# Performance work log

Measured on AMD Instinct MI355X. Metric: run time of the kernel, lower is better.

## Reference

```python
import jax, jax.numpy as jnp
import numpy as np

N = 100000
E = 3200000
IN_CH, HID, OUT = 256, 64, 32


def setup_inputs() -> dict:
    key = jax.random.key(0)
    ks = jax.random.split(key, 8)
    x = jax.random.normal(ks[0], (N, IN_CH), dtype=jnp.float32)
    edge_index = jax.random.randint(ks[1], (2, E), 0, N, dtype=jnp.int64)
    # Glorot-ish init for weights, zeros for biases (PyG GCNConv: lin has no bias; conv bias added post-aggregation)
    W1 = jax.random.normal(ks[2], (IN_CH, HID), dtype=jnp.float32) / np.sqrt(IN_CH)
    b1 = jnp.zeros((HID,), dtype=jnp.float32)
    W2 = jax.random.normal(ks[3], (HID, OUT), dtype=jnp.float32) / np.sqrt(HID)
    b2 = jnp.zeros((OUT,), dtype=jnp.float32)
    Wc = jax.random.normal(ks[4], (OUT, 1), dtype=jnp.float32) / np.sqrt(OUT)
    bc = jnp.zeros((1,), dtype=jnp.float32)
    return {"x": x, "edge_index": edge_index, "W1": W1, "b1": b1,
            "W2": W2, "b2": b2, "Wc": Wc, "bc": bc}


def _gcn_norm(edge_index, num_nodes):
    # Add self-loops (PyG default), compute symmetric normalization D^{-1/2} A D^{-1/2}
    loops = jnp.arange(num_nodes, dtype=edge_index.dtype)
    row = jnp.concatenate([edge_index[0], loops])  # source
    col = jnp.concatenate([edge_index[1], loops])  # target (aggregation index)
    ones = jnp.ones(row.shape[0], dtype=jnp.float32)
    deg = jax.ops.segment_sum(ones, col, num_segments=num_nodes)
    dis = jnp.where(deg > 0, jax.lax.rsqrt(jnp.maximum(deg, 1e-12)), 0.0)
    norm = dis[row] * dis[col]  # [E+N]
    return row, col, norm


def _gcn_conv(x, W, b, row, col, norm, num_nodes):
    h = x @ W                                   # [N, F_out] dense transform first
    msg = h[row] * norm[:, None]                # gather + scale per edge
    agg = jax.ops.segment_sum(msg, col, num_segments=num_nodes)
    return agg + b


def reference(x, edge_index, W1, b1, W2, b2, Wc, bc):
    num_nodes = x.shape[0]
    row, col, norm = _gcn_norm(edge_index, num_nodes)
    h = jax.nn.elu(_gcn_conv(x, W1, b1, row, col, norm, num_nodes))
    h = jax.nn.elu(_gcn_conv(h, W2, b2, row, col, norm, num_nodes))
    return (h @ Wc + bc)[:, 0]                  # squeeze(1) -> [N]
```

## Files before the change

kernel.cpp:

```cpp
#include <hip/hip_runtime.h>
#include <hip/hip_fp16.h>
#include <math.h>

#define N_NODES 100000
#define N_EDGES 3200000
#define IN_CH   256
#define HID     64
#define OUTC    32
#define BSHIFT  8
#define BNODES  256
#define NBUCK   ((N_NODES + BNODES - 1) / BNODES)
#define CHUNK   4096
#define EPT     16
#define CAP     9216

static constexpr size_t align256(size_t x) { return (x + 255) & ~(size_t)255; }
static constexpr size_t OFF_PTRB = 0;
static constexpr size_t OFF_PTRE = OFF_PTRB + align256((size_t)N_NODES * 4);
static constexpr size_t OFF_GCUR = OFF_PTRE + align256((size_t)N_NODES * 4);
static constexpr size_t OFF_DIS  = OFF_GCUR + align256((size_t)NBUCK * 4);
static constexpr size_t OFF_SRC  = OFF_DIS  + align256((size_t)N_NODES * 4);
static constexpr size_t OFF_PART = OFF_SRC  + align256((size_t)NBUCK * CAP * 4);
static constexpr size_t OFF_S1   = OFF_PART;
static constexpr size_t OFF_S2   = OFF_PART + align256((size_t)NBUCK * CAP * 4);

typedef _Float16 f16;
typedef f16 f16x8 __attribute__((ext_vector_type(8)));
typedef float f32x4 __attribute__((ext_vector_type(4)));

__device__ __forceinline__ void acc8(float* acc, float4 raw) {
    const __half2* hp = (const __half2*)&raw;
    float2 f0 = __half22float2(hp[0]);
    float2 f1 = __half22float2(hp[1]);
    float2 f2 = __half22float2(hp[2]);
    float2 f3 = __half22float2(hp[3]);
    acc[0] += f0.x; acc[1] += f0.y; acc[2] += f1.x; acc[3] += f1.y;
    acc[4] += f2.x; acc[5] += f2.y; acc[6] += f3.x; acc[7] += f3.y;
}

__global__ __launch_bounds__(256) void bucket_init(int* __restrict__ gcur) {
    int b = blockIdx.x * 256 + threadIdx.x;
    if (b < NBUCK) gcur[b] = b * CAP;
}

__global__ __launch_bounds__(256) void partition_edges(const int* __restrict__ row,
                                                       const int* __restrict__ col,
                                                       int* __restrict__ gcur,
                                                       int* __restrict__ part) {
    __shared__ int lhist[NBUCK];
    __shared__ int lbase[NBUCK];
    const int t  = threadIdx.x;
    const int e0 = blockIdx.x * CHUNK;
    for (int i = t; i < NBUCK; i += 256) lhist[i] = 0;
    __syncthreads();

    int pk[EPT], br[EPT];
#pragma unroll
    for (int i = 0; i < EPT; ++i) {
        int e = e0 + i * 256 + t;
        if (e < N_EDGES) {
            int d = col[e];
            int b = d >> BSHIFT;
            int r = atomicAdd(&lhist[b], 1);
            pk[i] = row[e] | ((d & (BNODES - 1)) << 17);
            br[i] = b | (r << 10);
        } else {
            br[i] = -1;
        }
    }
    __syncthreads();

    const int off = (int)((blockIdx.x * 131u) % NBUCK);
    for (int i = t; i < NBUCK; i += 256) {
        int bb = i + off;
        if (bb >= NBUCK) bb -= NBUCK;
        int c = lhist[bb];
        lbase[bb] = (c > 0) ? atomicAdd(&gcur[bb], c) : 0;
    }
    __syncthreads();

#pragma unroll
    for (int i = 0; i < EPT; ++i) {
        if (br[i] >= 0) {
            int b = br[i] & 1023;
            int r = br[i] >> 10;
            part[lbase[b] + r] = pk[i];
        }
    }
}

__global__ __launch_bounds__(256) void bucket_build(const int* __restrict__ gcur,
                                                    const int* __restrict__ part,
                                                    int* __restrict__ ptrb,
                                                    int* __restrict__ ptre,
                                                    float* __restrict__ dis,
                                                    int* __restrict__ srcs) {
    __shared__ int pcache[CAP];
    __shared__ int lh[BNODES];
    __shared__ int lb[BNODES];
    __shared__ int lcur[BNODES];
    __shared__ int ls[BNODES];
    const int b = blockIdx.x;
    const int t = threadIdx.x;
    lh[t] = 0; lcur[t] = 0;
    __syncthreads();
    const int cnt = gcur[b] - b * CAP;
    const size_t pbase = (size_t)b * CAP;

    for (int i = t; i < cnt; i += 256) {
        int p = part[pbase + i];
        pcache[i] = p;
        atomicAdd(&lh[p >> 17], 1);
    }
    __syncthreads();

    int val = lh[t];
    ls[t] = val;
    __syncthreads();
    for (int off = 1; off < BNODES; off <<= 1) {
        int add = (t >= off) ? ls[t - off] : 0;
        __syncthreads();
        ls[t] += add;
        __syncthreads();
    }
    lb[t] = ls[t] - val;
    __syncthreads();

    int v = b * BNODES + t;
    if (v < N_NODES) {
        ptrb[v] = b * CAP + lb[t];
        ptre[v] = b * CAP + lb[t] + val;
        dis[v]  = rsqrtf((float)val + 1.0f);
    }

    for (int i = t; i < cnt; i += 256) {
        int p    = pcache[i];
        int dlow = p >> 17;
        int src  = p & 0x1FFFF;
        int r    = atomicAdd(&lcur[dlow], 1);
        srcs[pbase + lb[dlow] + r] = src;
    }
}

__global__ __launch_bounds__(256) void gemm1(const float* __restrict__ x,
                                             const float* __restrict__ W1,
                                             const float* __restrict__ dis,
                                             __half* __restrict__ s1h) {
    __shared__ __align__(16) char lds_raw[30720];
    f16* xh  = (f16*)lds_raw;
    f16* xl  = (f16*)(lds_raw + 10240);
    f16* wth = (f16*)(lds_raw + 20480);
    f16* wtl = (f16*)(lds_raw + 25600);

    const int t    = threadIdx.x;
    const int row0 = blockIdx.x * 128;
    const int lane = t & 63;
    const int wv   = t >> 6;
    const int lr   = lane & 15;
    const int kg   = lane >> 4;

    f32x4 acc[2][4];
#pragma unroll
    for (int m = 0; m < 2; ++m)
#pragma unroll
        for (int n = 0; n < 4; ++n) acc[m][n] = (f32x4){0.f, 0.f, 0.f, 0.f};

    for (int kt = 0; kt < 8; ++kt) {
#pragma unroll
        for (int i = 0; i < 4; ++i) {
            int L  = i * 256 + t;
            int r  = L >> 3;
            int k4 = L & 7;
            int rg = row0 + r;
            float4 v = make_float4(0.f, 0.f, 0.f, 0.f);
            if (rg < N_NODES)
                v = ((const float4*)x)[(size_t)rg * 64 + kt * 8 + k4];
            union { f16 h[4]; unsigned long long u; } ph, pl;
            const float* vf = (const float*)&v;
#pragma unroll
            for (int c = 0; c < 4; ++c) {
                f16 hi = (f16)vf[c];
                ph.h[c] = hi;
                pl.h[c] = (f16)(vf[c] - (float)hi);
            }
            *(unsigned long long*)(&xh[r * 40 + k4 * 4]) = ph.u;
            *(unsigned long long*)(&xl[r * 40 + k4 * 4]) = pl.u;
        }
#pragma unroll
        for (int i = 0; i < 2; ++i) {
            int L  = i * 256 + t;
            int k  = L >> 4;
            int j4 = L & 15;
            float4 v = ((const float4*)W1)[(size_t)(kt * 32 + k) * 16 + j4];
            const float* vf = (const float*)&v;
#pragma unroll
            for (int c = 0; c < 4; ++c) {
                f16 hi = (f16)vf[c];
                wth[(j4 * 4 + c) * 40 + k] = hi;
                wtl[(j4 * 4 + c) * 40 + k] = (f16)(vf[c] - (float)hi);
            }
        }
        __syncthreads();

        f16x8 ah[2], al[2], bh[4], bl[4];
#pragma unroll
        for (int m = 0; m < 2; ++m) {
            ah[m] = *(const f16x8*)(&xh[(wv * 32 + m * 16 + lr) * 40 + kg * 8]);
            al[m] = *(const f16x8*)(&xl[(wv * 32 + m * 16 + lr) * 40 + kg * 8]);
        }
#pragma unroll
        for (int n = 0; n < 4; ++n) {
            bh[n] = *(const f16x8*)(&wth[(n * 16 + lr) * 40 + kg * 8]);
            bl[n] = *(const f16x8*)(&wtl[(n * 16 + lr) * 40 + kg * 8]);
        }
#pragma unroll
        for (int m = 0; m < 2; ++m)
#pragma unroll
            for (int n = 0; n < 4; ++n) {
                acc[m][n] = __builtin_amdgcn_mfma_f32_16x16x32_f16(ah[m], bh[n], acc[m][n], 0, 0, 0);
                acc[m][n] = __builtin_amdgcn_mfma_f32_16x16x32_f16(ah[m], bl[n], acc[m][n], 0, 0, 0);
                acc[m][n] = __builtin_amdgcn_mfma_f32_16x16x32_f16(al[m], bh[n], acc[m][n], 0, 0, 0);
            }
        __syncthreads();
    }

    f16* ob = (f16*)lds_raw;
#pragma unroll
    for (int m = 0; m < 2; ++m) {
#pragma unroll
        for (int r = 0; r < 4; ++r) {
            int rl = wv * 32 + m * 16 + kg * 4 + r;
            int rg = row0 + rl;
            float d = dis[rg < N_NODES ? rg : (N_NODES - 1)];
#pragma unroll
            for (int n = 0; n < 4; ++n)
                ob[rl * 72 + n * 16 + lr] = (f16)(acc[m][n][r] * d);
        }
    }
    __syncthreads();
#pragma unroll
    for (int i = 0; i < 4; ++i) {
        int L = i * 256 + t;
        int r = L >> 3;
        int sg = L & 7;
        int rg = row0 + r;
        if (rg < N_NODES) {
            f16x8 v = *(const f16x8*)(&ob[r * 72 + sg * 8]);
            *(f16x8*)(s1h + (size_t)rg * HID + sg * 8) = v;
        }
    }
}

__global__ __launch_bounds__(256) void gather1(const __half* __restrict__ s1h,
                                               const int* __restrict__ ptrb,
                                               const int* __restrict__ ptre,
                                               const int* __restrict__ srcs,
                                               const float* __restrict__ dis,
                                               const float* __restrict__ b1,
                                               const float* __restrict__ W2,
                                               __half* __restrict__ s2h) {
    __shared__ float w2lds[HID * OUTC];
    __shared__ float hbuf[4][HID];

    const int t = threadIdx.x;
    {
        float4* l4 = (float4*)w2lds;
        const float4* s4 = (const float4*)W2;
        l4[t] = s4[t];
        l4[256 + t] = s4[256 + t];
    }
    __syncthreads();

    const int j = t & 63;
    const int w = t >> 6;
    const int l = j & 31;
    const int h = j >> 5;
    const int v = __builtin_amdgcn_readfirstlane(blockIdx.x * 4 + w);
    const __half2* s12 = (const __half2*)s1h;

    float2 acc;
    {
        float2 self = __half22float2(s12[(v << 5) | l]);
        acc = (h == 0) ? self : make_float2(0.f, 0.f);
    }
    const int beg = ptrb[v];
    const int end = ptre[v];

    for (int base = beg; base < end; base += 64) {
        int mysrc = 0;
        if (base + j < end) mysrc = srcs[base + j];
        int nk = end - base;
        if (nk > 64) nk = 64;
        const int full = nk >> 1;
        int i = 0;
        for (; i + 8 <= full; i += 8) {
            int s  = 2 * i + h;
            int a0 = __shfl(mysrc, s,      64);
            int a1 = __shfl(mysrc, s + 2,  64);
            int a2 = __shfl(mysrc, s + 4,  64);
            int a3 = __shfl(mysrc, s + 6,  64);
            int a4 = __shfl(mysrc, s + 8,  64);
            int a5 = __shfl(mysrc, s + 10, 64);
            int a6 = __shfl(mysrc, s + 12, 64);
            int a7 = __shfl(mysrc, s + 14, 64);
            float2 g0 = __half22float2(s12[(a0 << 5) | l]);
            float2 g1 = __half22float2(s12[(a1 << 5) | l]);
            float2 g2 = __half22float2(s12[(a2 << 5) | l]);
            float2 g3 = __half22float2(s12[(a3 << 5) | l]);
            float2 g4 = __half22float2(s12[(a4 << 5) | l]);
            float2 g5 = __half22float2(s12[(a5 << 5) | l]);
            float2 g6 = __half22float2(s12[(a6 << 5) | l]);
            float2 g7 = __half22float2(s12[(a7 << 5) | l]);
            acc.x += ((g0.x + g1.x) + (g2.x + g3.x)) + ((g4.x + g5.x) + (g6.x + g7.x));
            acc.y += ((g0.y + g1.y) + (g2.y + g3.y)) + ((g4.y + g5.y) + (g6.y + g7.y));
        }
        if (2 * i < nk) {
            const int last = nk - 1;
#pragma unroll
            for (int u = 0; u < 8; ++u) {
                int s  = 2 * (i + u) + h;
                int sc = s < last ? s : last;
                int a  = __shfl(mysrc, sc, 64);
                float wgt = (s < nk) ? 1.f : 0.f;
                float2 g = __half22float2(s12[(a << 5) | l]);
                acc.x = fmaf(wgt, g.x, acc.x);
                acc.y = fmaf(wgt, g.y, acc.y);
            }
        }
    }
    acc.x += __shfl_xor(acc.x, 32, 64);
    acc.y += __shfl_xor(acc.y, 32, 64);

    float dv = dis[v];
    float2 bb = *(const float2*)(b1 + 2 * l);
    float t0 = dv * acc.x + bb.x;
    float t1 = dv * acc.y + bb.y;
    float h0 = t0 > 0.f ? t0 : (expf(t0) - 1.f);
    float h1 = t1 > 0.f ? t1 : (expf(t1) - 1.f);
    if (h == 0) {
        hbuf[w][2 * l]     = h0;
        hbuf[w][2 * l + 1] = h1;
    }

    const int jo = j & 31;
    const int kb = (j >> 5) * 32;
    float p = 0.f;
#pragma unroll
    for (int kk = 0; kk < 32; ++kk)
        p += hbuf[w][kb + kk] * w2lds[(kb + kk) * OUTC + jo];
    p += __shfl_xor(p, 32, 64);
    if (j < 32) {
        s2h[(size_t)v * OUTC + jo] = __float2half(dv * p);
    }
}

__global__ __launch_bounds__(256) void gather2(const __half* __restrict__ s2h,
                                               const int* __restrict__ ptrb,
                                               const int* __restrict__ ptre,
                                               const int* __restrict__ srcs,
                                               const float* __restrict__ dis,
                                               const float* __restrict__ b2,
                                               const float* __restrict__ Wc,
                                               const float* __restrict__ bc,
                                               float* __restrict__ out) {
    const int j = threadIdx.x & 63;
    const int w = threadIdx.x >> 6;
    const int l = j & 3;
    const int e = j >> 2;
    const int v = __builtin_amdgcn_readfirstlane(blockIdx.x * 4 + w);
    const float4* s24 = (const float4*)s2h;

    float acc[8] = {0.f, 0.f, 0.f, 0.f, 0.f, 0.f, 0.f, 0.f};
    if (e == 0) acc8(acc, s24[(v << 2) | l]);

    const int beg = ptrb[v];
    const int end = ptre[v];
    for (int base = beg; base < end; base += 64) {
        int mys = 0;
        if (base + j < end) mys = srcs[base + j];
        int nk = end - base;
        if (nk > 64) nk = 64;
        int off = 0;
        for (; off + 32 <= nk; off += 32) {
            int a0 = __shfl(mys, off + e,      64);
            int a1 = __shfl(mys, off + 16 + e, 64);
            float4 r0 = s24[(a0 << 2) | l];
            float4 r1 = s24[(a1 << 2) | l];
            acc8(acc, r0);
            acc8(acc, r1);
        }
        if (off < nk) {
            const int last = nk - 1;
            int s0 = off + e, s1 = off + 16 + e;
            int a0 = __shfl(mys, s0 < last ? s0 : last, 64);
            int a1 = __shfl(mys, s1 < last ? s1 : last, 64);
            if (s0 < nk) acc8(acc, s24[(a0 << 2) | l]);
            if (s1 < nk) acc8(acc, s24[(a1 << 2) | l]);
        }
    }
#pragma unroll
    for (int i = 0; i < 8; ++i) {
        acc[i] += __shfl_xor(acc[i], 4, 64);
        acc[i] += __shfl_xor(acc[i], 8, 64);
        acc[i] += __shfl_xor(acc[i], 16, 64);
        acc[i] += __shfl_xor(acc[i], 32, 64);
    }

    float dv = dis[v];
    float4 ba = ((const float4*)b2)[2 * l];
    float4 bb = ((const float4*)b2)[2 * l + 1];
    float4 wa = ((const float4*)Wc)[2 * l];
    float4 wb = ((const float4*)Wc)[2 * l + 1];
    const float* bf = (const float*)&ba;
    const float* bg = (const float*)&bb;
    const float* wf = (const float*)&wa;
    const float* wg = (const float*)&wb;
    float p = 0.f;
#pragma unroll
    for (int i = 0; i < 8; ++i) {
        float bias = (i < 4) ? bf[i] : bg[i - 4];
        float wc   = (i < 4) ? wf[i] : wg[i - 4];
        float tt = dv * acc[i] + bias;
        float hh = tt > 0.f ? tt : (expf(tt) - 1.f);
        p += hh * wc;
    }
    p += __shfl_xor(p, 1, 64);
    p += __shfl_xor(p, 2, 64);
    if (j == 0) out[v] = p + bc[0];
}

extern "C" void kernel_launch(void* const* d_in, const int* in_sizes, int n_in,
                              void* d_out, int out_size, void* d_ws, size_t ws_size,
                              hipStream_t stream) {
    const float* x  = (const float*)d_in[0];
    const int*   ei = (const int*)d_in[1];
    const float* W1 = (const float*)d_in[2];
    const float* b1 = (const float*)d_in[3];
    const float* W2 = (const float*)d_in[4];
    const float* b2 = (const float*)d_in[5];
    const float* Wc = (const float*)d_in[6];
    const float* bc = (const float*)d_in[7];
    float* out = (float*)d_out;

    const int* row = ei;
    const int* col = ei + N_EDGES;

    char* ws = (char*)d_ws;
    int*    ptrb = (int*)   (ws + OFF_PTRB);
    int*    ptre = (int*)   (ws + OFF_PTRE);
    int*    gcur = (int*)   (ws + OFF_GCUR);
    float*  dis  = (float*) (ws + OFF_DIS);
    int*    srcs = (int*)   (ws + OFF_SRC);
    int*    part = (int*)   (ws + OFF_PART);
    __half* s1h  = (__half*)(ws + OFF_S1);
    __half* s2h  = (__half*)(ws + OFF_S2);

    bucket_init    <<<(NBUCK + 255) / 256, 256, 0, stream>>>(gcur);
    partition_edges<<<(N_EDGES + CHUNK - 1) / CHUNK, 256, 0, stream>>>(row, col, gcur, part);
    bucket_build   <<<NBUCK, 256, 0, stream>>>(gcur, part, ptrb, ptre, dis, srcs);

    gemm1  <<<(N_NODES + 127) / 128, 256, 0, stream>>>(x, W1, dis, s1h);
    gather1<<<N_NODES / 4, 256, 0, stream>>>(s1h, ptrb, ptre, srcs, dis, b1, W2, s2h);
    gather2<<<N_NODES / 4, 256, 0, stream>>>(s2h, ptrb, ptre, srcs, dis, b2, Wc, bc, out);
}
```

Baseline: 375.1 us.

## Fuse edge partitioning and first GEMM into one interleaved launch

```diff
diff --git a/kernel.cpp b/kernel.cpp
--- a/kernel.cpp
+++ b/kernel.cpp
@@ -13,6 +13,8 @@
 #define CHUNK   4096
 #define EPT     16
 #define CAP     9216
+#define NPART   ((N_EDGES + CHUNK - 1) / CHUNK)
+#define NG1     ((N_NODES + 127) / 128)
 
 static constexpr size_t align256(size_t x) { return (x + 255) & ~(size_t)255; }
 static constexpr size_t OFF_PTRB = 0;
@@ -21,8 +23,8 @@
 static constexpr size_t OFF_DIS  = OFF_GCUR + align256((size_t)NBUCK * 4);
 static constexpr size_t OFF_SRC  = OFF_DIS  + align256((size_t)N_NODES * 4);
 static constexpr size_t OFF_PART = OFF_SRC  + align256((size_t)NBUCK * CAP * 4);
-static constexpr size_t OFF_S1   = OFF_PART;
-static constexpr size_t OFF_S2   = OFF_PART + align256((size_t)NBUCK * CAP * 4);
+static constexpr size_t OFF_S1   = OFF_PART + align256((size_t)NBUCK * CAP * 4);
+static constexpr size_t OFF_S2   = OFF_S1   + align256((size_t)N_NODES * HID * 2);
 
 typedef _Float16 f16;
 typedef f16 f16x8 __attribute__((ext_vector_type(8)));
@@ -38,19 +40,16 @@
     acc[4] += f2.x; acc[5] += f2.y; acc[6] += f3.x; acc[7] += f3.y;
 }
 
-__global__ __launch_bounds__(256) void bucket_init(int* __restrict__ gcur) {
-    int b = blockIdx.x * 256 + threadIdx.x;
-    if (b < NBUCK) gcur[b] = b * CAP;
-}
-
-__global__ __launch_bounds__(256) void partition_edges(const int* __restrict__ row,
-                                                       const int* __restrict__ col,
-                                                       int* __restrict__ gcur,
-                                                       int* __restrict__ part) {
-    __shared__ int lhist[NBUCK];
-    __shared__ int lbase[NBUCK];
+
+__device__ __forceinline__ void partition_body(int pb, const int* __restrict__ row,
+                                               const int* __restrict__ col,
+                                               int* __restrict__ gcur,
+                                               int* __restrict__ part,
+                                               char* smem) {
+    int* lhist = (int*)smem;
+    int* lbase = lhist + NBUCK;
     const int t  = threadIdx.x;
-    const int e0 = blockIdx.x * CHUNK;
+    const int e0 = pb * CHUNK;
     for (int i = t; i < NBUCK; i += 256) lhist[i] = 0;
     __syncthreads();
 
@@ -70,7 +69,7 @@
     }
     __syncthreads();
 
-    const int off = (int)((blockIdx.x * 131u) % NBUCK);
+    const int off = (int)((pb * 131u) % NBUCK);
     for (int i = t; i < NBUCK; i += 256) {
         int bb = i + off;
         if (bb >= NBUCK) bb -= NBUCK;
@@ -84,9 +83,128 @@
         if (br[i] >= 0) {
             int b = br[i] & 1023;
             int r = br[i] >> 10;
-            part[lbase[b] + r] = pk[i];
-        }
-    }
+            part[b * CAP + lbase[b] + r] = pk[i];
+        }
+    }
+}
+
+__device__ __forceinline__ void gemm1_body(int gb, const float* __restrict__ x,
+                                           const float* __restrict__ W1,
+                                           __half* __restrict__ s1h,
+                                           char* lds_raw) {
+    f16* xh  = (f16*)lds_raw;
+    f16* xl  = (f16*)(lds_raw + 10240);
+    f16* wth = (f16*)(lds_raw + 20480);
+    f16* wtl = (f16*)(lds_raw + 25600);
+
+    const int t    = threadIdx.x;
+    const int row0 = gb * 128;
+    const int lane = t & 63;
+    const int wv   = t >> 6;
+    const int lr   = lane & 15;
+    const int kg   = lane >> 4;
+
+    f32x4 acc[2][4];
+#pragma unroll
+    for (int m = 0; m < 2; ++m)
+#pragma unroll
+        for (int n = 0; n < 4; ++n) acc[m][n] = (f32x4){0.f, 0.f, 0.f, 0.f};
+
+    for (int kt = 0; kt < 8; ++kt) {
+#pragma unroll
+        for (int i = 0; i < 4; ++i) {
+            int L  = i * 256 + t;
+            int r  = L >> 3;
+            int k4 = L & 7;
+            int rg = row0 + r;
+            float4 v = make_float4(0.f, 0.f, 0.f, 0.f);
+            if (rg < N_NODES)
+                v = ((const float4*)x)[(size_t)rg * 64 + kt * 8 + k4];
+            union { f16 h[4]; unsigned long long u; } ph, pl;
+            const float* vf = (const float*)&v;
+#pragma unroll
+            for (int c = 0; c < 4; ++c) {
+                f16 hi = (f16)vf[c];
+                ph.h[c] = hi;
+                pl.h[c] = (f16)(vf[c] - (float)hi);
+            }
+            *(unsigned long long*)(&xh[r * 40 + k4 * 4]) = ph.u;
+            *(unsigned long long*)(&xl[r * 40 + k4 * 4]) = pl.u;
+        }
+#pragma unroll
+        for (int i = 0; i < 2; ++i) {
+            int L  = i * 256 + t;
+            int k  = L >> 4;
+            int j4 = L & 15;
+            float4 v = ((const float4*)W1)[(size_t)(kt * 32 + k) * 16 + j4];
+            const float* vf = (const float*)&v;
+#pragma unroll
+            for (int c = 0; c < 4; ++c) {
+                f16 hi = (f16)vf[c];
+                wth[(j4 * 4 + c) * 40 + k] = hi;
+                wtl[(j4 * 4 + c) * 40 + k] = (f16)(vf[c] - (float)hi);
+            }
+        }
+        __syncthreads();
+
+        f16x8 ah[2], al[2], bh[4], bl[4];
+#pragma unroll
+        for (int m = 0; m < 2; ++m) {
+            ah[m] = *(const f16x8*)(&xh[(wv * 32 + m * 16 + lr) * 40 + kg * 8]);
+            al[m] = *(const f16x8*)(&xl[(wv * 32 + m * 16 + lr) * 40 + kg * 8]);
+        }
+#pragma unroll
+        for (int n = 0; n < 4; ++n) {
+            bh[n] = *(const f16x8*)(&wth[(n * 16 + lr) * 40 + kg * 8]);
+            bl[n] = *(const f16x8*)(&wtl[(n * 16 + lr) * 40 + kg * 8]);
+        }
+#pragma unroll
+        for (int m = 0; m < 2; ++m)
+#pragma unroll
+            for (int n = 0; n < 4; ++n) {
+                acc[m][n] = __builtin_amdgcn_mfma_f32_16x16x32_f16(ah[m], bh[n], acc[m][n], 0, 0, 0);
+                acc[m][n] = __builtin_amdgcn_mfma_f32_16x16x32_f16(ah[m], bl[n], acc[m][n], 0, 0, 0);
+                acc[m][n] = __builtin_amdgcn_mfma_f32_16x16x32_f16(al[m], bh[n], acc[m][n], 0, 0, 0);
+            }
+        __syncthreads();
+    }
+
+    f16* ob = (f16*)lds_raw;
+#pragma unroll
+    for (int m = 0; m < 2; ++m) {
+#pragma unroll
+        for (int r = 0; r < 4; ++r) {
+            int rl = wv * 32 + m * 16 + kg * 4 + r;
+#pragma unroll
+            for (int n = 0; n < 4; ++n)
+                ob[rl * 72 + n * 16 + lr] = (f16)(acc[m][n][r]);
+        }
+    }
+    __syncthreads();
+#pragma unroll
+    for (int i = 0; i < 4; ++i) {
+        int L = i * 256 + t;
+        int r = L >> 3;
+        int sg = L & 7;
+        int rg = row0 + r;
+        if (rg < N_NODES) {
+            f16x8 v = *(const f16x8*)(&ob[r * 72 + sg * 8]);
+            *(f16x8*)(s1h + (size_t)rg * HID + sg * 8) = v;
+        }
+    }
+}
+
+__global__ __launch_bounds__(256) void fused_pg(const int* __restrict__ row,
+                                                const int* __restrict__ col,
+                                                int* __restrict__ gcur,
+                                                int* __restrict__ part,
+                                                const float* __restrict__ x,
+                                                const float* __restrict__ W1,
+                                                __half* __restrict__ s1h) {
+    __shared__ __align__(16) char smem[30720];
+    const int bid = blockIdx.x;
+    if (bid & 1) gemm1_body(bid >> 1, x, W1, s1h, smem);
+    else         partition_body(bid >> 1, row, col, gcur, part, smem);
 }
 
 __global__ __launch_bounds__(256) void bucket_build(const int* __restrict__ gcur,
@@ -104,7 +222,7 @@
     const int t = threadIdx.x;
     lh[t] = 0; lcur[t] = 0;
     __syncthreads();
-    const int cnt = gcur[b] - b * CAP;
+    const int cnt = gcur[b];
     const size_t pbase = (size_t)b * CAP;
 
     for (int i = t; i < cnt; i += 256) {
@@ -139,115 +257,6 @@
         int src  = p & 0x1FFFF;
         int r    = atomicAdd(&lcur[dlow], 1);
         srcs[pbase + lb[dlow] + r] = src;
-    }
-}
-
-__global__ __launch_bounds__(256) void gemm1(const float* __restrict__ x,
-                                             const float* __restrict__ W1,
-                                             const float* __restrict__ dis,
-                                             __half* __restrict__ s1h) {
-    __shared__ __align__(16) char lds_raw[30720];
-    f16* xh  = (f16*)lds_raw;
-    f16* xl  = (f16*)(lds_raw + 10240);
-    f16* wth = (f16*)(lds_raw + 20480);
-    f16* wtl = (f16*)(lds_raw + 25600);
-
-    const int t    = threadIdx.x;
-    const int row0 = blockIdx.x * 128;
-    const int lane = t & 63;
-    const int wv   = t >> 6;
-    const int lr   = lane & 15;
-    const int kg   = lane >> 4;
-
-    f32x4 acc[2][4];
-#pragma unroll
-    for (int m = 0; m < 2; ++m)
-#pragma unroll
-        for (int n = 0; n < 4; ++n) acc[m][n] = (f32x4){0.f, 0.f, 0.f, 0.f};
-
-    for (int kt = 0; kt < 8; ++kt) {
-#pragma unroll
-        for (int i = 0; i < 4; ++i) {
-            int L  = i * 256 + t;
-            int r  = L >> 3;
-            int k4 = L & 7;
-            int rg = row0 + r;
-            float4 v = make_float4(0.f, 0.f, 0.f, 0.f);
-            if (rg < N_NODES)
-                v = ((const float4*)x)[(size_t)rg * 64 + kt * 8 + k4];
-            union { f16 h[4]; unsigned long long u; } ph, pl;
-            const float* vf = (const float*)&v;
-#pragma unroll
-            for (int c = 0; c < 4; ++c) {
-                f16 hi = (f16)vf[c];
-                ph.h[c] = hi;
-                pl.h[c] = (f16)(vf[c] - (float)hi);
-            }
-            *(unsigned long long*)(&xh[r * 40 + k4 * 4]) = ph.u;
-            *(unsigned long long*)(&xl[r * 40 + k4 * 4]) = pl.u;
-        }
-#pragma unroll
-        for (int i = 0; i < 2; ++i) {
-            int L  = i * 256 + t;
-            int k  = L >> 4;
-            int j4 = L & 15;
-            float4 v = ((const float4*)W1)[(size_t)(kt * 32 + k) * 16 + j4];
-            const float* vf = (const float*)&v;
-#pragma unroll
-            for (int c = 0; c < 4; ++c) {
-                f16 hi = (f16)vf[c];
-                wth[(j4 * 4 + c) * 40 + k] = hi;
-                wtl[(j4 * 4 + c) * 40 + k] = (f16)(vf[c] - (float)hi);
-            }
-        }
-        __syncthreads();
-
-        f16x8 ah[2], al[2], bh[4], bl[4];
-#pragma unroll
-        for (int m = 0; m < 2; ++m) {
-            ah[m] = *(const f16x8*)(&xh[(wv * 32 + m * 16 + lr) * 40 + kg * 8]);
-            al[m] = *(const f16x8*)(&xl[(wv * 32 + m * 16 + lr) * 40 + kg * 8]);
-        }
-#pragma unroll
-        for (int n = 0; n < 4; ++n) {
-            bh[n] = *(const f16x8*)(&wth[(n * 16 + lr) * 40 + kg * 8]);
-            bl[n] = *(const f16x8*)(&wtl[(n * 16 + lr) * 40 + kg * 8]);
-        }
-#pragma unroll
-        for (int m = 0; m < 2; ++m)
-#pragma unroll
-            for (int n = 0; n < 4; ++n) {
-                acc[m][n] = __builtin_amdgcn_mfma_f32_16x16x32_f16(ah[m], bh[n], acc[m][n], 0, 0, 0);
-                acc[m][n] = __builtin_amdgcn_mfma_f32_16x16x32_f16(ah[m], bl[n], acc[m][n], 0, 0, 0);
-                acc[m][n] = __builtin_amdgcn_mfma_f32_16x16x32_f16(al[m], bh[n], acc[m][n], 0, 0, 0);
-            }
-        __syncthreads();
-    }
-
-    f16* ob = (f16*)lds_raw;
-#pragma unroll
-    for (int m = 0; m < 2; ++m) {
-#pragma unroll
-        for (int r = 0; r < 4; ++r) {
-            int rl = wv * 32 + m * 16 + kg * 4 + r;
-            int rg = row0 + rl;
-            float d = dis[rg < N_NODES ? rg : (N_NODES - 1)];
-#pragma unroll
-            for (int n = 0; n < 4; ++n)
-                ob[rl * 72 + n * 16 + lr] = (f16)(acc[m][n][r] * d);
-        }
-    }
-    __syncthreads();
-#pragma unroll
-    for (int i = 0; i < 4; ++i) {
-        int L = i * 256 + t;
-        int r = L >> 3;
-        int sg = L & 7;
-        int rg = row0 + r;
-        if (rg < N_NODES) {
-            f16x8 v = *(const f16x8*)(&ob[r * 72 + sg * 8]);
-            *(f16x8*)(s1h + (size_t)rg * HID + sg * 8) = v;
-        }
     }
 }
 
@@ -278,10 +287,12 @@
     const int v = __builtin_amdgcn_readfirstlane(blockIdx.x * 4 + w);
     const __half2* s12 = (const __half2*)s1h;
 
+    const float dv = dis[v];
     float2 acc;
     {
         float2 self = __half22float2(s12[(v << 5) | l]);
-        acc = (h == 0) ? self : make_float2(0.f, 0.f);
+        acc = (h == 0) ? make_float2(self.x * dv, self.y * dv)
+                       : make_float2(0.f, 0.f);
     }
     const int beg = ptrb[v];
     const int end = ptre[v];
@@ -303,6 +314,8 @@
             int a5 = __shfl(mysrc, s + 10, 64);
             int a6 = __shfl(mysrc, s + 12, 64);
             int a7 = __shfl(mysrc, s + 14, 64);
+            float d0 = dis[a0], d1 = dis[a1], d2 = dis[a2], d3 = dis[a3];
+            float d4 = dis[a4], d5 = dis[a5], d6 = dis[a6], d7 = dis[a7];
             float2 g0 = __half22float2(s12[(a0 << 5) | l]);
             float2 g1 = __half22float2(s12[(a1 << 5) | l]);
             float2 g2 = __half22float2(s12[(a2 << 5) | l]);
@@ -311,8 +324,14 @@
             float2 g5 = __half22float2(s12[(a5 << 5) | l]);
             float2 g6 = __half22float2(s12[(a6 << 5) | l]);
             float2 g7 = __half22float2(s12[(a7 << 5) | l]);
-            acc.x += ((g0.x + g1.x) + (g2.x + g3.x)) + ((g4.x + g5.x) + (g6.x + g7.x));
-            acc.y += ((g0.y + g1.y) + (g2.y + g3.y)) + ((g4.y + g5.y) + (g6.y + g7.y));
+            acc.x = fmaf(d0, g0.x, acc.x); acc.y = fmaf(d0, g0.y, acc.y);
+            acc.x = fmaf(d1, g1.x, acc.x); acc.y = fmaf(d1, g1.y, acc.y);
+            acc.x = fmaf(d2, g2.x, acc.x); acc.y = fmaf(d2, g2.y, acc.y);
+            acc.x = fmaf(d3, g3.x, acc.x); acc.y = fmaf(d3, g3.y, acc.y);
+            acc.x = fmaf(d4, g4.x, acc.x); acc.y = fmaf(d4, g4.y, acc.y);
+            acc.x = fmaf(d5, g5.x, acc.x); acc.y = fmaf(d5, g5.y, acc.y);
+            acc.x = fmaf(d6, g6.x, acc.x); acc.y = fmaf(d6, g6.y, acc.y);
+            acc.x = fmaf(d7, g7.x, acc.x); acc.y = fmaf(d7, g7.y, acc.y);
         }
         if (2 * i < nk) {
             const int last = nk - 1;
@@ -321,7 +340,7 @@
                 int s  = 2 * (i + u) + h;
                 int sc = s < last ? s : last;
                 int a  = __shfl(mysrc, sc, 64);
-                float wgt = (s < nk) ? 1.f : 0.f;
+                float wgt = (s < nk) ? dis[a] : 0.f;
                 float2 g = __half22float2(s12[(a << 5) | l]);
                 acc.x = fmaf(wgt, g.x, acc.x);
                 acc.y = fmaf(wgt, g.y, acc.y);
@@ -331,7 +350,6 @@
     acc.x += __shfl_xor(acc.x, 32, 64);
     acc.y += __shfl_xor(acc.y, 32, 64);
 
-    float dv = dis[v];
     float2 bb = *(const float2*)(b1 + 2 * l);
     float t0 = dv * acc.x + bb.x;
     float t1 = dv * acc.y + bb.y;
@@ -455,11 +473,10 @@
     __half* s1h  = (__half*)(ws + OFF_S1);
     __half* s2h  = (__half*)(ws + OFF_S2);
 
-    bucket_init    <<<(NBUCK + 255) / 256, 256, 0, stream>>>(gcur);
-    partition_edges<<<(N_EDGES + CHUNK - 1) / CHUNK, 256, 0, stream>>>(row, col, gcur, part);
-    bucket_build   <<<NBUCK, 256, 0, stream>>>(gcur, part, ptrb, ptre, dis, srcs);
-
-    gemm1  <<<(N_NODES + 127) / 128, 256, 0, stream>>>(x, W1, dis, s1h);
+    hipMemsetAsync(gcur, 0, (size_t)NBUCK * 4, stream);
+    fused_pg    <<<NPART + NG1, 256, 0, stream>>>(row, col, gcur, part, x, W1, s1h);
+    bucket_build<<<NBUCK, 256, 0, stream>>>(gcur, part, ptrb, ptre, dis, srcs);
+
     gather1<<<N_NODES / 4, 256, 0, stream>>>(s1h, ptrb, ptre, srcs, dis, b1, W2, s2h);
     gather2<<<N_NODES / 4, 256, 0, stream>>>(s2h, ptrb, ptre, srcs, dis, b2, Wc, bc, out);
 }
```

Measured after the change: 367.3 us. 2.1% less time.
